# Performance work log

Hardware: AMD Instinct MI355X
Metric: run time of the kernel (lower is better)

Reference implementation:

```python
import jax, jax.numpy as jnp
import numpy as np

N, E, IN, HID, OUT = 100000, 1000000, 64, 64, 40


def setup_inputs() -> dict:
    key = jax.random.key(0)
    ks = jax.random.split(key, 8)
    x = jax.random.normal(ks[0], (N, IN), dtype=jnp.float32)
    edge_index = jax.random.randint(ks[1], (2, E), 0, N, dtype=jnp.int32)
    # Glorot-ish scaled weights
    W1l = jax.random.normal(ks[2], (IN, HID), jnp.float32) / np.sqrt(IN)
    W1r = jax.random.normal(ks[3], (IN, HID), jnp.float32) / np.sqrt(IN)
    b1 = jnp.zeros((HID,), jnp.float32)
    W2l = jax.random.normal(ks[4], (HID, OUT), jnp.float32) / np.sqrt(HID)
    W2r = jax.random.normal(ks[5], (HID, OUT), jnp.float32) / np.sqrt(HID)
    b2 = jnp.zeros((OUT,), jnp.float32)
    return {"x": x, "edge_index": edge_index, "W1l": W1l, "W1r": W1r,
            "b1": b1, "W2l": W2l, "W2r": W2r, "b2": b2}


def sage_conv(x, src, dst, Wl, Wr, b, n):
    # PyG SAGEConv (mean aggr): out = lin_l(mean_{j in N(i)} x_j) + lin_r(x_i)
    msg = x[src]                                              # [E, d] gather
    agg = jax.ops.segment_sum(msg, dst, num_segments=n)      # [n, d] scatter-add
    deg = jax.ops.segment_sum(jnp.ones((src.shape[0],), x.dtype), dst,
                              num_segments=n)                # in-degree
    agg = agg / jnp.maximum(deg, 1.0)[:, None]               # mean; 0 for isolated nodes
    return agg @ Wl + x @ Wr + b


def reference(x, edge_index, W1l, W1r, b1, W2l, W2r, b2):
    n = x.shape[0]
    src, dst = edge_index[0], edge_index[1]
    h = jax.nn.relu(sage_conv(x, src, dst, W1l, W1r, b1, n))
    # dropout is identity in eval mode (training=False)
    return sage_conv(h, src, dst, W2l, W2r, b2, n)
```

## Files before the change

### kernel.cpp

```cpp
#include <hip/hip_runtime.h>

#define NN 100000
#define EE 1000000
#define NR 256
#define RSZ 391
#define CAP2 8192

typedef unsigned short ushort_t;
typedef short bf16x8 __attribute__((ext_vector_type(8)));
typedef float f32x4 __attribute__((ext_vector_type(4)));
typedef int   i32x4 __attribute__((ext_vector_type(4)));

__device__ __forceinline__ unsigned short f2bf(float f) {
    unsigned u = __builtin_bit_cast(unsigned, f);
    u += 0x7fffu + ((u >> 16) & 1u);
    return (unsigned short)(u >> 16);
}
__device__ __forceinline__ float bflo(unsigned u) {
    return __builtin_bit_cast(float, u << 16);
}
__device__ __forceinline__ float bfhi(unsigned u) {
    return __builtin_bit_cast(float, u & 0xffff0000u);
}
__device__ __forceinline__ unsigned pk2(float a, float b) {
    return (unsigned)f2bf(a) | ((unsigned)f2bf(b) << 16);
}

__global__ __launch_bounds__(256) void k_cast(
    const float* __restrict__ x, ushort_t* __restrict__ xb,
    int* __restrict__ seg_cnt)
{
    if (blockIdx.x == 0) seg_cnt[threadIdx.x] = 0;
    size_t t = (size_t)blockIdx.x * 256 + threadIdx.x;
    const float4 v0 = *reinterpret_cast<const float4*>(x + t * 8);
    const float4 v1 = *reinterpret_cast<const float4*>(x + t * 8 + 4);
    uint4 r;
    r.x = pk2(v0.x, v0.y); r.y = pk2(v0.z, v0.w);
    r.z = pk2(v1.x, v1.y); r.w = pk2(v1.z, v1.w);
    *reinterpret_cast<uint4*>(xb + t * 8) = r;
}

__global__ __launch_bounds__(256) void k_part(
    const int* __restrict__ ei, int* __restrict__ seg_cnt, int2* __restrict__ seg)
{
    __shared__ int cnt[NR];
    __shared__ int basech[NR];
    const int t  = threadIdx.x;
    const int e0 = (blockIdx.x * 256 + t) * 16;
    cnt[t] = 0;
    __syncthreads();

    int d[16], s[16];
    int nval = 0;
    if (e0 + 15 < EE) {
        #pragma unroll
        for (int q = 0; q < 4; ++q) {
            const i32x4 dv = __builtin_nontemporal_load(
                reinterpret_cast<const i32x4*>(ei + EE + e0 + q * 4));
            const i32x4 sv = __builtin_nontemporal_load(
                reinterpret_cast<const i32x4*>(ei + e0 + q * 4));
            d[q*4+0]=dv.x; d[q*4+1]=dv.y; d[q*4+2]=dv.z; d[q*4+3]=dv.w;
            s[q*4+0]=sv.x; s[q*4+1]=sv.y; s[q*4+2]=sv.z; s[q*4+3]=sv.w;
        }
        nval = 16;
    } else {
        for (int j = 0; j < 16 && e0 + j < EE; ++j) {
            d[j] = ei[EE + e0 + j]; s[j] = ei[e0 + j]; ++nval;
        }
    }
    for (int j = 0; j < nval; ++j) atomicAdd(&cnt[d[j] / RSZ], 1);
    __syncthreads();
    basech[t] = t * CAP2 + atomicAdd(seg_cnt + t, cnt[t]);
    cnt[t] = 0;
    __syncthreads();
    for (int j = 0; j < nval; ++j) {
        const int r = d[j] / RSZ;
        const int o = atomicAdd(&cnt[r], 1);
        const int addr = basech[r] + o;
        if (addr < (r + 1) * CAP2)
            seg[addr] = make_int2(d[j], s[j]);
    }
}

__global__ __launch_bounds__(NR) void k_scanR(
    const int* __restrict__ seg_cnt, int* __restrict__ roff,
    int* __restrict__ rowptr)
{
    __shared__ int part[NR];
    const int t = threadIdx.x;
    const int v = min(seg_cnt[t], CAP2);
    part[t] = v;
    __syncthreads();
    for (int off = 1; off < NR; off <<= 1) {
        int u = (t >= off) ? part[t - off] : 0;
        __syncthreads();
        part[t] += u;
        __syncthreads();
    }
    roff[t] = part[t] - v;
    if (t == NR - 1) { roff[NR] = part[t]; rowptr[NN] = part[t]; }
}

__global__ __launch_bounds__(256) void k_sortB(
    const int2* __restrict__ seg, const int* __restrict__ seg_cnt,
    const int* __restrict__ roff, int* __restrict__ rowptr,
    int* __restrict__ srcs)
{
    const int r     = blockIdx.x;
    const int n0    = r * RSZ;
    const int n1    = min(n0 + RSZ, NN);
    const int nrg   = n1 - n0;
    const int sbase = r * CAP2;
    const int m     = min(seg_cnt[r], CAP2);
    const int obase = roff[r];
    const int t     = threadIdx.x;

    __shared__ int cur[RSZ + 1];
    __shared__ int part[256];
    __shared__ int lsr[CAP2];

    for (int i = t; i < nrg; i += 256) cur[i] = 0;
    __syncthreads();
    for (int i = t; i < m; i += 256) {
        const int2 q = seg[sbase + i];
        const int loc = q.x - n0;
        if (loc >= 0 && loc < nrg) atomicAdd(&cur[loc], 1);
    }
    __syncthreads();
    const int i0 = 2 * t, i1 = 2 * t + 1;
    const int e0 = (i0 < nrg) ? cur[i0] : 0;
    const int e1 = (i1 < nrg) ? cur[i1] : 0;
    const int s  = e0 + e1;
    part[t] = s;
    __syncthreads();
    for (int off = 1; off < 256; off <<= 1) {
        int u = (t >= off) ? part[t - off] : 0;
        __syncthreads();
        part[t] += u;
        __syncthreads();
    }
    const int ex = part[t] - s;
    __syncthreads();
    if (i0 < nrg) { rowptr[n0 + i0] = obase + ex;      cur[i0] = ex; }
    if (i1 < nrg) { rowptr[n0 + i1] = obase + ex + e0; cur[i1] = ex + e0; }
    __syncthreads();
    for (int i = t; i < m; i += 256) {
        const int2 q = seg[sbase + i];
        const int loc = q.x - n0;
        if (loc >= 0 && loc < nrg) {
            const int pos = atomicAdd(&cur[loc], 1);
            if (pos < CAP2) lsr[pos] = q.y;
        }
    }
    __syncthreads();
    for (int i = t; i < m; i += 256)
        srcs[obase + i] = lsr[i];
}

__global__ __launch_bounds__(256, 8) void k_gather1(
    const ushort_t* __restrict__ rows, const int* __restrict__ rowptr,
    const int* __restrict__ srcs, ushort_t* __restrict__ aggm)
{
    const int lane = threadIdx.x & 63;
    const int w    = threadIdx.x >> 6;
    const int p    = lane & 7;
    const int gb   = lane & 56;
    const int node = blockIdx.x * 32 + w * 8 + (lane >> 3);

    const int beg = rowptr[node];
    const int nb  = rowptr[node + 1] - beg;

    float a0=0,a1=0,a2=0,a3=0,a4=0,a5=0,a6=0,a7=0;
    for (int j0 = 0; j0 < nb; j0 += 8) {
        const int cnt = min(nb - j0, 8);
        const int idx = (p < cnt) ? __builtin_nontemporal_load(srcs + beg + j0 + p) : 0;
        int t = 0;
        for (; t + 3 < cnt; t += 4) {
            int s0 = __shfl(idx, gb + t),     s1 = __shfl(idx, gb + t + 1);
            int s2 = __shfl(idx, gb + t + 2), s3 = __shfl(idx, gb + t + 3);
            const uint4 v0 = *reinterpret_cast<const uint4*>(rows + (size_t)s0 * 64 + p * 8);
            const uint4 v1 = *reinterpret_cast<const uint4*>(rows + (size_t)s1 * 64 + p * 8);
            const uint4 v2 = *reinterpret_cast<const uint4*>(rows + (size_t)s2 * 64 + p * 8);
            const uint4 v3 = *reinterpret_cast<const uint4*>(rows + (size_t)s3 * 64 + p * 8);
            a0 += bflo(v0.x)+bflo(v1.x)+bflo(v2.x)+bflo(v3.x);
            a1 += bfhi(v0.x)+bfhi(v1.x)+bfhi(v2.x)+bfhi(v3.x);
            a2 += bflo(v0.y)+bflo(v1.y)+bflo(v2.y)+bflo(v3.y);
            a3 += bfhi(v0.y)+bfhi(v1.y)+bfhi(v2.y)+bfhi(v3.y);
            a4 += bflo(v0.z)+bflo(v1.z)+bflo(v2.z)+bflo(v3.z);
            a5 += bfhi(v0.z)+bfhi(v1.z)+bfhi(v2.z)+bfhi(v3.z);
            a6 += bflo(v0.w)+bflo(v1.w)+bflo(v2.w)+bflo(v3.w);
            a7 += bfhi(v0.w)+bfhi(v1.w)+bfhi(v2.w)+bfhi(v3.w);
        }
        for (; t < cnt; ++t) {
            int s = __shfl(idx, gb + t);
            const uint4 v = *reinterpret_cast<const uint4*>(rows + (size_t)s * 64 + p * 8);
            a0 += bflo(v.x); a1 += bfhi(v.x); a2 += bflo(v.y); a3 += bfhi(v.y);
            a4 += bflo(v.z); a5 += bfhi(v.z); a6 += bflo(v.w); a7 += bfhi(v.w);
        }
    }
    const float inv = 1.0f / (float)max(nb, 1);
    uint4 r;
    r.x = pk2(a0*inv, a1*inv); r.y = pk2(a2*inv, a3*inv);
    r.z = pk2(a4*inv, a5*inv); r.w = pk2(a6*inv, a7*inv);
    *reinterpret_cast<uint4*>(aggm + (size_t)node * 64 + p * 8) = r;
}

__global__ __launch_bounds__(256) void k_dense1(
    const ushort_t* __restrict__ xb, const ushort_t* __restrict__ aggm_b,
    const float* __restrict__ W1l, const float* __restrict__ W1r,
    const float* __restrict__ b1,  const float* __restrict__ W2l,
    const float* __restrict__ W2r, const float* __restrict__ b2,
    ushort_t* __restrict__ hW2b, float* __restrict__ base)
{
    __shared__ __align__(16) ushort_t sW1T[64 * 136];
    __shared__ __align__(16) ushort_t sW2T[80 * 72];
    __shared__ __align__(16) ushort_t sH[4][16 * 72];
    __shared__ float sB1[64];
    __shared__ float sB2[40];

    const int t = threadIdx.x;
    {
        const int n = t & 63, kr = t >> 6;
        for (int i = 0; i < 32; ++i) {
            int k = kr * 32 + i;
            float v = (k < 64) ? W1l[k * 64 + n] : W1r[(k - 64) * 64 + n];
            sW1T[n * 136 + k] = f2bf(v);
        }
    }
    for (int idx = t; idx < 80 * 64; idx += 256) {
        int n2 = idx % 80, k = idx / 80;
        float v = (n2 < 40) ? W2l[k * 40 + n2] : W2r[k * 40 + (n2 - 40)];
        sW2T[n2 * 72 + k] = f2bf(v);
    }
    if (t < 64) sB1[t] = b1[t];
    if (t < 40) sB2[t] = b2[t];
    __syncthreads();

    const int w = t >> 6, lane = t & 63;
    const int l15 = lane & 15, g = lane >> 4;
    const int nbase = blockIdx.x * 64 + w * 16;
    const int arow = min(nbase + l15, NN - 1);

    const f32x4 zero = {0.f, 0.f, 0.f, 0.f};
    f32x4 acc0 = zero, acc1 = zero, acc2_ = zero, acc3 = zero;
    bf16x8 afr[4];
    #pragma unroll
    for (int ks = 0; ks < 4; ++ks) {
        const int k0 = ks * 32;
        const ushort_t* src = (k0 < 64)
            ? (aggm_b + (size_t)arow * 64 + k0 + 8 * g)
            : (xb     + (size_t)arow * 64 + (k0 - 64) + 8 * g);
        afr[ks] = *reinterpret_cast<const bf16x8*>(src);
    }
    #pragma unroll
    for (int ks = 0; ks < 4; ++ks) {
        const bf16x8 b0  = *reinterpret_cast<const bf16x8*>(&sW1T[( 0 + l15) * 136 + ks * 32 + 8 * g]);
        const bf16x8 b1f = *reinterpret_cast<const bf16x8*>(&sW1T[(16 + l15) * 136 + ks * 32 + 8 * g]);
        const bf16x8 b2f = *reinterpret_cast<const bf16x8*>(&sW1T[(32 + l15) * 136 + ks * 32 + 8 * g]);
        const bf16x8 b3f = *reinterpret_cast<const bf16x8*>(&sW1T[(48 + l15) * 136 + ks * 32 + 8 * g]);
        acc0  = __builtin_amdgcn_mfma_f32_16x16x32_bf16(afr[ks], b0,  acc0,  0, 0, 0);
        acc1  = __builtin_amdgcn_mfma_f32_16x16x32_bf16(afr[ks], b1f, acc1,  0, 0, 0);
        acc2_ = __builtin_amdgcn_mfma_f32_16x16x32_bf16(afr[ks], b2f, acc2_, 0, 0, 0);
        acc3  = __builtin_amdgcn_mfma_f32_16x16x32_bf16(afr[ks], b3f, acc3,  0, 0, 0);
    }

    {
        const float bb0 = sB1[ 0 + l15], bb1 = sB1[16 + l15];
        const float bb2 = sB1[32 + l15], bb3 = sB1[48 + l15];
        #pragma unroll
        for (int r = 0; r < 4; ++r) {
            const int row = g * 4 + r;
            sH[w][row * 72 +  0 + l15] = f2bf(fmaxf(acc0[r]  + bb0, 0.f));
            sH[w][row * 72 + 16 + l15] = f2bf(fmaxf(acc1[r]  + bb1, 0.f));
            sH[w][row * 72 + 32 + l15] = f2bf(fmaxf(acc2_[r] + bb2, 0.f));
            sH[w][row * 72 + 48 + l15] = f2bf(fmaxf(acc3[r]  + bb3, 0.f));
        }
    }
    __syncthreads();

    bf16x8 a2[2];
    a2[0] = *reinterpret_cast<const bf16x8*>(&sH[w][l15 * 72 +  0 + 8 * g]);
    a2[1] = *reinterpret_cast<const bf16x8*>(&sH[w][l15 * 72 + 32 + 8 * g]);
    f32x4 o[5] = {zero, zero, zero, zero, zero};
    #pragma unroll
    for (int nt = 0; nt < 5; ++nt) {
        #pragma unroll
        for (int ks = 0; ks < 2; ++ks) {
            const bf16x8 bfr = *reinterpret_cast<const bf16x8*>(
                &sW2T[(nt * 16 + l15) * 72 + ks * 32 + 8 * g]);
            o[nt] = __builtin_amdgcn_mfma_f32_16x16x32_bf16(a2[ks], bfr, o[nt], 0, 0, 0);
        }
    }

    #pragma unroll
    for (int nt = 0; nt < 5; ++nt) {
        const int f2 = nt * 16 + l15;
        #pragma unroll
        for (int r = 0; r < 4; ++r) {
            const int node = nbase + g * 4 + r;
            if (node < NN) {
                const float v = o[nt][r];
                if (f2 < 64)
                    hW2b[(size_t)node * 64 + f2] = (f2 < 40) ? f2bf(v) : (ushort_t)0;
                if (f2 >= 40)
                    base[(size_t)node * 40 + (f2 - 40)] = v + sB2[f2 - 40];
            }
        }
    }
}

__global__ __launch_bounds__(256, 8) void k_gather2(
    const ushort_t* __restrict__ rows, const int* __restrict__ rowptr,
    const int* __restrict__ srcs, const float* __restrict__ base,
    float* __restrict__ out)
{
    const int lane = threadIdx.x & 63;
    const int w    = threadIdx.x >> 6;
    const int p    = lane & 7;
    const int gb   = lane & 56;
    const int node = blockIdx.x * 32 + w * 8 + (lane >> 3);

    const int beg = rowptr[node];
    const int nb  = rowptr[node + 1] - beg;

    float a0=0,a1=0,a2=0,a3=0,a4=0,a5=0,a6=0,a7=0;
    for (int j0 = 0; j0 < nb; j0 += 8) {
        const int cnt = min(nb - j0, 8);
        const int idx = (p < cnt) ? __builtin_nontemporal_load(srcs + beg + j0 + p) : 0;
        int t = 0;
        for (; t + 3 < cnt; t += 4) {
            int s0 = __shfl(idx, gb + t),     s1 = __shfl(idx, gb + t + 1);
            int s2 = __shfl(idx, gb + t + 2), s3 = __shfl(idx, gb + t + 3);
            const uint4 v0 = *reinterpret_cast<const uint4*>(rows + (size_t)s0 * 64 + p * 8);
            const uint4 v1 = *reinterpret_cast<const uint4*>(rows + (size_t)s1 * 64 + p * 8);
            const uint4 v2 = *reinterpret_cast<const uint4*>(rows + (size_t)s2 * 64 + p * 8);
            const uint4 v3 = *reinterpret_cast<const uint4*>(rows + (size_t)s3 * 64 + p * 8);
            a0 += bflo(v0.x)+bflo(v1.x)+bflo(v2.x)+bflo(v3.x);
            a1 += bfhi(v0.x)+bfhi(v1.x)+bfhi(v2.x)+bfhi(v3.x);
            a2 += bflo(v0.y)+bflo(v1.y)+bflo(v2.y)+bflo(v3.y);
            a3 += bfhi(v0.y)+bfhi(v1.y)+bfhi(v2.y)+bfhi(v3.y);
            a4 += bflo(v0.z)+bflo(v1.z)+bflo(v2.z)+bflo(v3.z);
            a5 += bfhi(v0.z)+bfhi(v1.z)+bfhi(v2.z)+bfhi(v3.z);
            a6 += bflo(v0.w)+bflo(v1.w)+bflo(v2.w)+bflo(v3.w);
            a7 += bfhi(v0.w)+bfhi(v1.w)+bfhi(v2.w)+bfhi(v3.w);
        }
        for (; t < cnt; ++t) {
            int s = __shfl(idx, gb + t);
            const uint4 v = *reinterpret_cast<const uint4*>(rows + (size_t)s * 64 + p * 8);
            a0 += bflo(v.x); a1 += bfhi(v.x); a2 += bflo(v.y); a3 += bfhi(v.y);
            a4 += bflo(v.z); a5 += bfhi(v.z); a6 += bflo(v.w); a7 += bfhi(v.w);
        }
    }
    if (p < 5) {
        const float inv = 1.0f / (float)max(nb, 1);
        const float4 bb0 = *reinterpret_cast<const float4*>(base + (size_t)node * 40 + p * 8);
        const float4 bb1 = *reinterpret_cast<const float4*>(base + (size_t)node * 40 + p * 8 + 4);
        float4 r0, r1;
        r0.x = a0*inv + bb0.x; r0.y = a1*inv + bb0.y; r0.z = a2*inv + bb0.z; r0.w = a3*inv + bb0.w;
        r1.x = a4*inv + bb1.x; r1.y = a5*inv + bb1.y; r1.z = a6*inv + bb1.z; r1.w = a7*inv + bb1.w;
        *reinterpret_cast<float4*>(out + (size_t)node * 40 + p * 8)     = r0;
        *reinterpret_cast<float4*>(out + (size_t)node * 40 + p * 8 + 4) = r1;
    }
}

extern "C" void kernel_launch(void* const* d_in, const int* in_sizes, int n_in,
                              void* d_out, int out_size, void* d_ws, size_t ws_size,
                              hipStream_t stream) {
    const float* x   = (const float*)d_in[0];
    const int*   ei  = (const int*)  d_in[1];
    const float* W1l = (const float*)d_in[2];
    const float* W1r = (const float*)d_in[3];
    const float* b1  = (const float*)d_in[4];
    const float* W2l = (const float*)d_in[5];
    const float* W2r = (const float*)d_in[6];
    const float* b2  = (const float*)d_in[7];
    float* out = (float*)d_out;

    int* wsi = (int*)d_ws;
    int* seg_cnt = wsi;
    int* roff    = wsi + NR;
    int* rowptr  = wsi + 2 * NR + 2;
    int* srcs    = rowptr + NN + 8;
    int2* seg    = (int2*)(srcs + EE + ((NN + EE) & 1 ? 1 : 0) + 1);
    ushort_t* xb     = (ushort_t*)(seg + (size_t)NR * CAP2);
    ushort_t* aggm_b = xb     + (size_t)NN * 64;
    ushort_t* hW2b   = aggm_b + (size_t)NN * 64;
    float*    base   = (float*)(hW2b + (size_t)NN * 64);

    k_cast<<<NN * 64 / 8 / 256, 256, 0, stream>>>(x, xb, seg_cnt);
    k_part<<<(EE + 4095) / 4096, 256, 0, stream>>>(ei, seg_cnt, seg);
    k_scanR<<<1, NR, 0, stream>>>(seg_cnt, roff, rowptr);
    k_sortB<<<NR, 256, 0, stream>>>(seg, seg_cnt, roff, rowptr, srcs);
    k_gather1<<<NN / 32, 256, 0, stream>>>(xb, rowptr, srcs, aggm_b);
    k_dense1<<<(NN + 63) / 64, 256, 0, stream>>>(xb, aggm_b, W1l, W1r, b1,
                                                 W2l, W2r, b2, hW2b, base);
    k_gather2<<<NN / 32, 256, 0, stream>>>(hW2b, rowptr, srcs, base, out);
}
```

Before: 126.9 us.

## Fold scan into sort kernel, loop dense tiles per block, compact hW2 rows

```diff
diff --git a/kernel.cpp b/kernel.cpp
--- a/kernel.cpp
+++ b/kernel.cpp
@@ -82,42 +82,34 @@
     }
 }
 
-__global__ __launch_bounds__(NR) void k_scanR(
-    const int* __restrict__ seg_cnt, int* __restrict__ roff,
-    int* __restrict__ rowptr)
-{
-    __shared__ int part[NR];
-    const int t = threadIdx.x;
-    const int v = min(seg_cnt[t], CAP2);
-    part[t] = v;
-    __syncthreads();
-    for (int off = 1; off < NR; off <<= 1) {
-        int u = (t >= off) ? part[t - off] : 0;
-        __syncthreads();
-        part[t] += u;
-        __syncthreads();
-    }
-    roff[t] = part[t] - v;
-    if (t == NR - 1) { roff[NR] = part[t]; rowptr[NN] = part[t]; }
-}
-
 __global__ __launch_bounds__(256) void k_sortB(
     const int2* __restrict__ seg, const int* __restrict__ seg_cnt,
-    const int* __restrict__ roff, int* __restrict__ rowptr,
-    int* __restrict__ srcs)
+    int* __restrict__ rowptr, int* __restrict__ srcs)
 {
     const int r     = blockIdx.x;
     const int n0    = r * RSZ;
     const int n1    = min(n0 + RSZ, NN);
     const int nrg   = n1 - n0;
     const int sbase = r * CAP2;
+    const int t     = threadIdx.x;
+
+    __shared__ int cur[RSZ + 1];
+    __shared__ int part[NR];
+    __shared__ int lsr[CAP2];
+
+    const int vc = min(seg_cnt[t], CAP2);
+    part[t] = vc;
+    __syncthreads();
+    for (int off = 1; off < NR; off <<= 1) {
+        int u = (t >= off) ? part[t - off] : 0;
+        __syncthreads();
+        part[t] += u;
+        __syncthreads();
+    }
     const int m     = min(seg_cnt[r], CAP2);
-    const int obase = roff[r];
-    const int t     = threadIdx.x;
-
-    __shared__ int cur[RSZ + 1];
-    __shared__ int part[256];
-    __shared__ int lsr[CAP2];
+    const int obase = part[r] - m;
+    if (r == NR - 1 && t == NR - 1) rowptr[NN] = part[t];
+    __syncthreads();
 
     for (int i = t; i < nrg; i += 256) cur[i] = 0;
     __syncthreads();
@@ -238,72 +230,76 @@
 
     const int w = t >> 6, lane = t & 63;
     const int l15 = lane & 15, g = lane >> 4;
-    const int nbase = blockIdx.x * 64 + w * 16;
-    const int arow = min(nbase + l15, NN - 1);
-
     const f32x4 zero = {0.f, 0.f, 0.f, 0.f};
-    f32x4 acc0 = zero, acc1 = zero, acc2_ = zero, acc3 = zero;
-    bf16x8 afr[4];
-    #pragma unroll
-    for (int ks = 0; ks < 4; ++ks) {
-        const int k0 = ks * 32;
-        const ushort_t* src = (k0 < 64)
-            ? (aggm_b + (size_t)arow * 64 + k0 + 8 * g)
-            : (xb     + (size_t)arow * 64 + (k0 - 64) + 8 * g);
-        afr[ks] = *reinterpret_cast<const bf16x8*>(src);
-    }
-    #pragma unroll
-    for (int ks = 0; ks < 4; ++ks) {
-        const bf16x8 b0  = *reinterpret_cast<const bf16x8*>(&sW1T[( 0 + l15) * 136 + ks * 32 + 8 * g]);
-        const bf16x8 b1f = *reinterpret_cast<const bf16x8*>(&sW1T[(16 + l15) * 136 + ks * 32 + 8 * g]);
-        const bf16x8 b2f = *reinterpret_cast<const bf16x8*>(&sW1T[(32 + l15) * 136 + ks * 32 + 8 * g]);
-        const bf16x8 b3f = *reinterpret_cast<const bf16x8*>(&sW1T[(48 + l15) * 136 + ks * 32 + 8 * g]);
-        acc0  = __builtin_amdgcn_mfma_f32_16x16x32_bf16(afr[ks], b0,  acc0,  0, 0, 0);
-        acc1  = __builtin_amdgcn_mfma_f32_16x16x32_bf16(afr[ks], b1f, acc1,  0, 0, 0);
-        acc2_ = __builtin_amdgcn_mfma_f32_16x16x32_bf16(afr[ks], b2f, acc2_, 0, 0, 0);
-        acc3  = __builtin_amdgcn_mfma_f32_16x16x32_bf16(afr[ks], b3f, acc3,  0, 0, 0);
-    }
-
-    {
-        const float bb0 = sB1[ 0 + l15], bb1 = sB1[16 + l15];
-        const float bb2 = sB1[32 + l15], bb3 = sB1[48 + l15];
-        #pragma unroll
-        for (int r = 0; r < 4; ++r) {
-            const int row = g * 4 + r;
-            sH[w][row * 72 +  0 + l15] = f2bf(fmaxf(acc0[r]  + bb0, 0.f));
-            sH[w][row * 72 + 16 + l15] = f2bf(fmaxf(acc1[r]  + bb1, 0.f));
-            sH[w][row * 72 + 32 + l15] = f2bf(fmaxf(acc2_[r] + bb2, 0.f));
-            sH[w][row * 72 + 48 + l15] = f2bf(fmaxf(acc3[r]  + bb3, 0.f));
-        }
-    }
-    __syncthreads();
-
-    bf16x8 a2[2];
-    a2[0] = *reinterpret_cast<const bf16x8*>(&sH[w][l15 * 72 +  0 + 8 * g]);
-    a2[1] = *reinterpret_cast<const bf16x8*>(&sH[w][l15 * 72 + 32 + 8 * g]);
-    f32x4 o[5] = {zero, zero, zero, zero, zero};
-    #pragma unroll
-    for (int nt = 0; nt < 5; ++nt) {
-        #pragma unroll
-        for (int ks = 0; ks < 2; ++ks) {
-            const bf16x8 bfr = *reinterpret_cast<const bf16x8*>(
-                &sW2T[(nt * 16 + l15) * 72 + ks * 32 + 8 * g]);
-            o[nt] = __builtin_amdgcn_mfma_f32_16x16x32_bf16(a2[ks], bfr, o[nt], 0, 0, 0);
-        }
-    }
-
-    #pragma unroll
-    for (int nt = 0; nt < 5; ++nt) {
-        const int f2 = nt * 16 + l15;
-        #pragma unroll
-        for (int r = 0; r < 4; ++r) {
-            const int node = nbase + g * 4 + r;
-            if (node < NN) {
-                const float v = o[nt][r];
-                if (f2 < 64)
-                    hW2b[(size_t)node * 64 + f2] = (f2 < 40) ? f2bf(v) : (ushort_t)0;
-                if (f2 >= 40)
-                    base[(size_t)node * 40 + (f2 - 40)] = v + sB2[f2 - 40];
+
+    for (int it = 0; it < 4; ++it) {
+        const int nbase = blockIdx.x * 256 + w * 64 + it * 16;
+        const int arow  = min(nbase + l15, NN - 1);
+
+        f32x4 acc0 = zero, acc1 = zero, acc2_ = zero, acc3 = zero;
+        bf16x8 afr[4];
+        #pragma unroll
+        for (int ks = 0; ks < 4; ++ks) {
+            const int k0 = ks * 32;
+            const ushort_t* src = (k0 < 64)
+                ? (aggm_b + (size_t)arow * 64 + k0 + 8 * g)
+                : (xb     + (size_t)arow * 64 + (k0 - 64) + 8 * g);
+            afr[ks] = *reinterpret_cast<const bf16x8*>(src);
+        }
+        #pragma unroll
+        for (int ks = 0; ks < 4; ++ks) {
+            const bf16x8 b0  = *reinterpret_cast<const bf16x8*>(&sW1T[( 0 + l15) * 136 + ks * 32 + 8 * g]);
+            const bf16x8 b1f = *reinterpret_cast<const bf16x8*>(&sW1T[(16 + l15) * 136 + ks * 32 + 8 * g]);
+            const bf16x8 b2f = *reinterpret_cast<const bf16x8*>(&sW1T[(32 + l15) * 136 + ks * 32 + 8 * g]);
+            const bf16x8 b3f = *reinterpret_cast<const bf16x8*>(&sW1T[(48 + l15) * 136 + ks * 32 + 8 * g]);
+            acc0  = __builtin_amdgcn_mfma_f32_16x16x32_bf16(afr[ks], b0,  acc0,  0, 0, 0);
+            acc1  = __builtin_amdgcn_mfma_f32_16x16x32_bf16(afr[ks], b1f, acc1,  0, 0, 0);
+            acc2_ = __builtin_amdgcn_mfma_f32_16x16x32_bf16(afr[ks], b2f, acc2_, 0, 0, 0);
+            acc3  = __builtin_amdgcn_mfma_f32_16x16x32_bf16(afr[ks], b3f, acc3,  0, 0, 0);
+        }
+
+        {
+            const float bb0 = sB1[ 0 + l15], bb1 = sB1[16 + l15];
+            const float bb2 = sB1[32 + l15], bb3 = sB1[48 + l15];
+            #pragma unroll
+            for (int r = 0; r < 4; ++r) {
+                const int row = g * 4 + r;
+                sH[w][row * 72 +  0 + l15] = f2bf(fmaxf(acc0[r]  + bb0, 0.f));
+                sH[w][row * 72 + 16 + l15] = f2bf(fmaxf(acc1[r]  + bb1, 0.f));
+                sH[w][row * 72 + 32 + l15] = f2bf(fmaxf(acc2_[r] + bb2, 0.f));
+                sH[w][row * 72 + 48 + l15] = f2bf(fmaxf(acc3[r]  + bb3, 0.f));
+            }
+        }
+        __syncthreads();
+
+        bf16x8 a2[2];
+        a2[0] = *reinterpret_cast<const bf16x8*>(&sH[w][l15 * 72 +  0 + 8 * g]);
+        a2[1] = *reinterpret_cast<const bf16x8*>(&sH[w][l15 * 72 + 32 + 8 * g]);
+        f32x4 o[5] = {zero, zero, zero, zero, zero};
+        #pragma unroll
+        for (int nt = 0; nt < 5; ++nt) {
+            #pragma unroll
+            for (int ks = 0; ks < 2; ++ks) {
+                const bf16x8 bfr = *reinterpret_cast<const bf16x8*>(
+                    &sW2T[(nt * 16 + l15) * 72 + ks * 32 + 8 * g]);
+                o[nt] = __builtin_amdgcn_mfma_f32_16x16x32_bf16(a2[ks], bfr, o[nt], 0, 0, 0);
+            }
+        }
+        __syncthreads();
+
+        #pragma unroll
+        for (int nt = 0; nt < 5; ++nt) {
+            const int f2 = nt * 16 + l15;
+            #pragma unroll
+            for (int r = 0; r < 4; ++r) {
+                const int node = nbase + g * 4 + r;
+                if (node < NN) {
+                    const float v = o[nt][r];
+                    if (f2 < 40)
+                        hW2b[(size_t)node * 40 + f2] = f2bf(v);
+                    if (f2 >= 40)
+                        base[(size_t)node * 40 + (f2 - 40)] = v + sB2[f2 - 40];
+                }
             }
         }
     }
@@ -331,24 +327,28 @@
         for (; t + 3 < cnt; t += 4) {
             int s0 = __shfl(idx, gb + t),     s1 = __shfl(idx, gb + t + 1);
             int s2 = __shfl(idx, gb + t + 2), s3 = __shfl(idx, gb + t + 3);
-            const uint4 v0 = *reinterpret_cast<const uint4*>(rows + (size_t)s0 * 64 + p * 8);
-            const uint4 v1 = *reinterpret_cast<const uint4*>(rows + (size_t)s1 * 64 + p * 8);
-            const uint4 v2 = *reinterpret_cast<const uint4*>(rows + (size_t)s2 * 64 + p * 8);
-            const uint4 v3 = *reinterpret_cast<const uint4*>(rows + (size_t)s3 * 64 + p * 8);
-            a0 += bflo(v0.x)+bflo(v1.x)+bflo(v2.x)+bflo(v3.x);
-            a1 += bfhi(v0.x)+bfhi(v1.x)+bfhi(v2.x)+bfhi(v3.x);
-            a2 += bflo(v0.y)+bflo(v1.y)+bflo(v2.y)+bflo(v3.y);
-            a3 += bfhi(v0.y)+bfhi(v1.y)+bfhi(v2.y)+bfhi(v3.y);
-            a4 += bflo(v0.z)+bflo(v1.z)+bflo(v2.z)+bflo(v3.z);
-            a5 += bfhi(v0.z)+bfhi(v1.z)+bfhi(v2.z)+bfhi(v3.z);
-            a6 += bflo(v0.w)+bflo(v1.w)+bflo(v2.w)+bflo(v3.w);
-            a7 += bfhi(v0.w)+bfhi(v1.w)+bfhi(v2.w)+bfhi(v3.w);
+            if (p < 5) {
+                const uint4 v0 = *reinterpret_cast<const uint4*>(rows + (size_t)s0 * 40 + p * 8);
+                const uint4 v1 = *reinterpret_cast<const uint4*>(rows + (size_t)s1 * 40 + p * 8);
+                const uint4 v2 = *reinterpret_cast<const uint4*>(rows + (size_t)s2 * 40 + p * 8);
+                const uint4 v3 = *reinterpret_cast<const uint4*>(rows + (size_t)s3 * 40 + p * 8);
+                a0 += bflo(v0.x)+bflo(v1.x)+bflo(v2.x)+bflo(v3.x);
+                a1 += bfhi(v0.x)+bfhi(v1.x)+bfhi(v2.x)+bfhi(v3.x);
+                a2 += bflo(v0.y)+bflo(v1.y)+bflo(v2.y)+bflo(v3.y);
+                a3 += bfhi(v0.y)+bfhi(v1.y)+bfhi(v2.y)+bfhi(v3.y);
+                a4 += bflo(v0.z)+bflo(v1.z)+bflo(v2.z)+bflo(v3.z);
+                a5 += bfhi(v0.z)+bfhi(v1.z)+bfhi(v2.z)+bfhi(v3.z);
+                a6 += bflo(v0.w)+bflo(v1.w)+bflo(v2.w)+bflo(v3.w);
+                a7 += bfhi(v0.w)+bfhi(v1.w)+bfhi(v2.w)+bfhi(v3.w);
+            }
         }
         for (; t < cnt; ++t) {
             int s = __shfl(idx, gb + t);
-            const uint4 v = *reinterpret_cast<const uint4*>(rows + (size_t)s * 64 + p * 8);
-            a0 += bflo(v.x); a1 += bfhi(v.x); a2 += bflo(v.y); a3 += bfhi(v.y);
-            a4 += bflo(v.z); a5 += bfhi(v.z); a6 += bflo(v.w); a7 += bfhi(v.w);
+            if (p < 5) {
+                const uint4 v = *reinterpret_cast<const uint4*>(rows + (size_t)s * 40 + p * 8);
+                a0 += bflo(v.x); a1 += bfhi(v.x); a2 += bflo(v.y); a3 += bfhi(v.y);
+                a4 += bflo(v.z); a5 += bfhi(v.z); a6 += bflo(v.w); a7 += bfhi(v.w);
+            }
         }
     }
     if (p < 5) {
@@ -378,21 +378,19 @@
 
     int* wsi = (int*)d_ws;
     int* seg_cnt = wsi;
-    int* roff    = wsi + NR;
-    int* rowptr  = wsi + 2 * NR + 2;
-    int* srcs    = rowptr + NN + 8;
-    int2* seg    = (int2*)(srcs + EE + ((NN + EE) & 1 ? 1 : 0) + 1);
+    int* rowptr  = wsi + NR;
+    int* srcs    = wsi + NR + NN + 8;
+    int2* seg    = (int2*)(srcs + EE);
     ushort_t* xb     = (ushort_t*)(seg + (size_t)NR * CAP2);
     ushort_t* aggm_b = xb     + (size_t)NN * 64;
     ushort_t* hW2b   = aggm_b + (size_t)NN * 64;
-    float*    base   = (float*)(hW2b + (size_t)NN * 64);
+    float*    base   = (float*)(hW2b + (size_t)NN * 40);
 
     k_cast<<<NN * 64 / 8 / 256, 256, 0, stream>>>(x, xb, seg_cnt);
     k_part<<<(EE + 4095) / 4096, 256, 0, stream>>>(ei, seg_cnt, seg);
-    k_scanR<<<1, NR, 0, stream>>>(seg_cnt, roff, rowptr);
-    k_sortB<<<NR, 256, 0, stream>>>(seg, seg_cnt, roff, rowptr, srcs);
+    k_sortB<<<NR, 256, 0, stream>>>(seg, seg_cnt, rowptr, srcs);
     k_gather1<<<NN / 32, 256, 0, stream>>>(xb, rowptr, srcs, aggm_b);
-    k_dense1<<<(NN + 63) / 64, 256, 0, stream>>>(xb, aggm_b, W1l, W1r, b1,
-                                                 W2l, W2r, b2, hW2b, base);
+    k_dense1<<<(NN + 255) / 256, 256, 0, stream>>>(xb, aggm_b, W1l, W1r, b1,
+                                                   W2l, W2r, b2, hW2b, base);
     k_gather2<<<NN / 32, 256, 0, stream>>>(hW2b, rowptr, srcs, base, out);
 }
```

After: 114.5 us. -9.8%, faster.
